# Kernel optimization log

Hardware: AMD Instinct MI355X
Metric: run time of the kernel (lower is better)

The kernel has to match this reference:

```python
import jax, jax.numpy as jnp
import numpy as np

DIM = 1024
NUM_HEADS = 16
HEAD_DIM = DIM // NUM_HEADS
SCALE = HEAD_DIM ** -0.5


def setup_inputs() -> dict:
    key = jax.random.key(0)
    k1, k2, k3 = jax.random.split(key, 3)
    B, S = 2, 2048
    x = jax.random.normal(k1, (B, S, DIM), dtype=jnp.float32)
    # nn.Linear(dim, 3*dim, bias=False): store as [in, out] for x @ W
    w_qkv = jax.random.normal(k2, (DIM, 3 * DIM), dtype=jnp.float32) * (DIM ** -0.5)
    w_out = jax.random.normal(k3, (DIM, DIM), dtype=jnp.float32) * (DIM ** -0.5)
    return {"x": x, "w_qkv": w_qkv, "w_out": w_out}


def reference(x, w_qkv, w_out):
    B, S, _ = x.shape
    qkv = x @ w_qkv                               # [B,S,3*D]
    q, k, v = jnp.split(qkv, 3, axis=-1)          # each [B,S,D]
    def heads(t):
        return t.reshape(B, S, NUM_HEADS, HEAD_DIM).transpose(0, 2, 1, 3)  # [B,H,S,d]
    q, k, v = heads(q), heads(k), heads(v)
    scores = jnp.einsum('bhqd,bhkd->bhqk', q, k) * SCALE   # [B,H,S,S]
    probs = jax.nn.softmax(scores, axis=-1)
    out = jnp.einsum('bhqk,bhkd->bhqd', probs, v)          # [B,H,S,d]
    out = out.transpose(0, 2, 1, 3).reshape(B, S, DIM)
    return out @ w_out
```

## Files before the change

### kernel.cpp

```cpp
#include <hip/hip_runtime.h>


typedef __bf16 bf16x8 __attribute__((ext_vector_type(8)));
typedef __bf16 bf16x4 __attribute__((ext_vector_type(4)));
typedef float floatx4 __attribute__((ext_vector_type(4)));

#define MFMA16(a, b, c) __builtin_amdgcn_mfma_f32_16x16x32_bf16((a), (b), (c), 0, 0, 0)

#if defined(__has_builtin)
#if __has_builtin(__builtin_amdgcn_exp2f)
#define EXP2F __builtin_amdgcn_exp2f
#endif
#endif
#ifndef EXP2F
#define EXP2F exp2f
#endif

__device__ __forceinline__ unsigned pk_bf16(float a, float b) {
  unsigned r;
  asm("v_cvt_pk_bf16_f32 %0, %1, %2" : "=v"(r) : "v"(a), "v"(b));
  return r;
}

__device__ __forceinline__ void gl_lds16(const void* g, void* l) {
  __builtin_amdgcn_global_load_lds((__attribute__((address_space(1))) void*)(g),
                                   (__attribute__((address_space(3))) void*)(l),
                                   16, 0, 0);
}

__global__ __launch_bounds__(256) void prep(const float* __restrict__ x,
                                            const float* __restrict__ w_qkv,
                                            const float* __restrict__ w_out,
                                            __bf16* __restrict__ xb,
                                            __bf16* __restrict__ wqkvt,
                                            __bf16* __restrict__ woutt) {
  __shared__ float tile[64][65];
  const int bid = blockIdx.x, t = threadIdx.x;
  if (bid < 4096) {
    int i = (bid * 256 + t) * 4;
    float4 v = *(const float4*)(x + i);
    bf16x4 o = { (__bf16)v.x, (__bf16)v.y, (__bf16)v.z, (__bf16)v.w };
    *(bf16x4*)(xb + i) = o;
    return;
  }
  const float* w;
  __bf16* wt;
  int K = 1024, N, k0, n0;
  if (bid < 4864) {
    int i = bid - 4096;
    w = w_qkv; wt = wqkvt; N = 3072; k0 = (i & 15) * 64; n0 = (i >> 4) * 64;
  } else {
    int i = bid - 4864;
    w = w_out; wt = woutt; N = 1024; k0 = (i & 15) * 64; n0 = (i >> 4) * 64;
  }
  for (int j = 0; j < 16; ++j) {
    int e = j * 256 + t, r = e >> 6, c = e & 63;
    tile[r][c] = w[(size_t)(k0 + r) * N + n0 + c];
  }
  __syncthreads();
  for (int j = 0; j < 16; ++j) {
    int e = j * 256 + t, r = e >> 6, c = e & 63;
    wt[(size_t)(n0 + r) * K + k0 + c] = (__bf16)tile[c][r];
  }
}

__global__ __launch_bounds__(256) void gemm_qkv(const __bf16* __restrict__ A,
                                                const __bf16* __restrict__ Bt,
                                                __bf16* __restrict__ qkb,
                                                __bf16* __restrict__ vt) {
  constexpr int K = 1024;
  constexpr float QSCALE = 0.18033688f;
  __shared__ __align__(16) __bf16 aS[128 * 32];
  __shared__ __align__(16) __bf16 bS[128 * 32];
  const int t = threadIdx.x;
  const int lane = t & 63, wave = t >> 6;
  const int l15 = lane & 15, quad = lane >> 4;
  const int wm = wave >> 1, wn = wave & 1;
  const int m0 = blockIdx.y * 128, n0 = blockIdx.x * 128;

  const floatx4 fzero = {0.f, 0.f, 0.f, 0.f};
  floatx4 acc[4][4];
  for (int mt = 0; mt < 4; ++mt)
    for (int nt = 0; nt < 4; ++nt) acc[mt][nt] = fzero;

  const int arow = t >> 2;
  const int ach = ((t & 3) ^ (arow & 3)) * 8;
  const __bf16* gA0 = A + (size_t)(m0 + arow) * K + ach;
  const __bf16* gA1 = gA0 + (size_t)64 * K;
  const __bf16* gB0 = Bt + (size_t)(n0 + arow) * K + ach;
  const __bf16* gB1 = gB0 + (size_t)64 * K;
  const int swz = (quad ^ (l15 & 3)) * 8;

  for (int k0 = 0; k0 < K; k0 += 32) {
    __syncthreads();
    gl_lds16(gA0 + k0, (char*)aS + t * 16);
    gl_lds16(gA1 + k0, (char*)aS + 4096 + t * 16);
    gl_lds16(gB0 + k0, (char*)bS + t * 16);
    gl_lds16(gB1 + k0, (char*)bS + 4096 + t * 16);
    __syncthreads();

    bf16x8 af[4], bfr[4];
    for (int mt = 0; mt < 4; ++mt)
      af[mt] = *(const bf16x8*)(aS + (wm * 64 + mt * 16 + l15) * 32 + swz);
    for (int nt = 0; nt < 4; ++nt)
      bfr[nt] = *(const bf16x8*)(bS + (wn * 64 + nt * 16 + l15) * 32 + swz);
    for (int mt = 0; mt < 4; ++mt)
      for (int nt = 0; nt < 4; ++nt)
        acc[mt][nt] = MFMA16(af[mt], bfr[nt], acc[mt][nt]);
  }

  for (int mt = 0; mt < 4; ++mt) {
    int row = m0 + wm * 64 + mt * 16 + quad * 4;
    for (int nt = 0; nt < 4; ++nt) {
      int col0 = n0 + wn * 64 + nt * 16;
      if (col0 >= 2048) {
        int dfull = col0 + l15 - 2048;
        int bh = ((row >> 11) << 4) + (dfull >> 6);
        int d = dfull & 63, s0 = row & 2047;
        bf16x4 pk = { (__bf16)acc[mt][nt][0], (__bf16)acc[mt][nt][1],
                      (__bf16)acc[mt][nt][2], (__bf16)acc[mt][nt][3] };
        *(bf16x4*)(vt + ((size_t)bh * 64 + d) * 2048 + s0) = pk;
      } else {
        float sc = (col0 < 1024) ? QSCALE : 1.0f;
        int col = col0 + l15;
        __bf16* cp = qkb + (size_t)row * 2048 + col;
        for (int r = 0; r < 4; ++r) cp[(size_t)r * 2048] = (__bf16)(acc[mt][nt][r] * sc);
      }
    }
  }
}

__global__ __launch_bounds__(256) void gemm_n64(const __bf16* __restrict__ A,
                                                const __bf16* __restrict__ Bt,
                                                float* __restrict__ C) {
  constexpr int K = 1024, N = 1024;
  __shared__ __align__(16) __bf16 aS[128 * 32];
  __shared__ __align__(16) __bf16 bS[64 * 32];
  const int t = threadIdx.x;
  const int lane = t & 63, wave = t >> 6;
  const int l15 = lane & 15, quad = lane >> 4;
  const int m0 = blockIdx.y * 128, n0 = blockIdx.x * 64;

  const floatx4 fzero = {0.f, 0.f, 0.f, 0.f};
  floatx4 acc[2][4];
  for (int mt = 0; mt < 2; ++mt)
    for (int nt = 0; nt < 4; ++nt) acc[mt][nt] = fzero;

  const int arow = t >> 2;
  const int ach = ((t & 3) ^ (arow & 3)) * 8;
  const __bf16* gA0 = A + (size_t)(m0 + arow) * K + ach;
  const __bf16* gA1 = gA0 + (size_t)64 * K;
  const __bf16* gB0 = Bt + (size_t)(n0 + arow) * K + ach;
  const int swz = (quad ^ (l15 & 3)) * 8;

  for (int k0 = 0; k0 < K; k0 += 32) {
    __syncthreads();
    gl_lds16(gA0 + k0, (char*)aS + t * 16);
    gl_lds16(gA1 + k0, (char*)aS + 4096 + t * 16);
    gl_lds16(gB0 + k0, (char*)bS + t * 16);
    __syncthreads();

    bf16x8 af[2], bfr[4];
    for (int mt = 0; mt < 2; ++mt)
      af[mt] = *(const bf16x8*)(aS + (wave * 32 + mt * 16 + l15) * 32 + swz);
    for (int nt = 0; nt < 4; ++nt)
      bfr[nt] = *(const bf16x8*)(bS + (nt * 16 + l15) * 32 + swz);
    for (int mt = 0; mt < 2; ++mt)
      for (int nt = 0; nt < 4; ++nt)
        acc[mt][nt] = MFMA16(af[mt], bfr[nt], acc[mt][nt]);
  }

  for (int mt = 0; mt < 2; ++mt) {
    int row = m0 + wave * 32 + mt * 16 + quad * 4;
    for (int nt = 0; nt < 4; ++nt) {
      int col = n0 + nt * 16 + l15;
      float* cp = C + (size_t)row * N + col;
      for (int r = 0; r < 4; ++r) cp[(size_t)r * N] = acc[mt][nt][r];
    }
  }
}

__global__ __launch_bounds__(256, 2) void flash_attn(const __bf16* __restrict__ qkb,
                                                     const __bf16* __restrict__ vt,
                                                     __bf16* __restrict__ out) {
  __shared__ __align__(16) __bf16 kS[2 * 64 * 64];
  __shared__ __align__(16) __bf16 vS[2 * 64 * 64];

  const int t = threadIdx.x;
  const int lane = t & 63, wave = t >> 6;
  const int l15 = lane & 15, quad = lane >> 4;
  const int id = blockIdx.x;
  const int xcd = id & 7, slot = id >> 3;
  const int bh = xcd * 4 + (slot >> 4), qb = slot & 15;
  const int b = bh >> 4, h = bh & 15;

  bf16x8 qf[2][2];
  for (int qt = 0; qt < 2; ++qt) {
    const __bf16* qp = qkb +
        (size_t)(b * 2048 + qb * 128 + wave * 32 + qt * 16 + l15) * 2048 + h * 64 + quad * 8;
    qf[qt][0] = *(const bf16x8*)qp;
    qf[qt][1] = *(const bf16x8*)(qp + 32);
  }

  bf16x8 onef;
  for (int j = 0; j < 8; ++j) onef[j] = (__bf16)1.0f;

  const floatx4 fzero = {0.f, 0.f, 0.f, 0.f};
  floatx4 oacc[2][4], lacc[2];
  for (int qt = 0; qt < 2; ++qt) {
    lacc[qt] = fzero;
    for (int dt = 0; dt < 4; ++dt) oacc[qt][dt] = fzero;
  }

  const int srow = t >> 3, schk = (t & 7) ^ (srow & 7);
  const __bf16* kg0 =
      qkb + (size_t)(b * 2048 + srow) * 2048 + 1024 + h * 64 + schk * 8;
  const __bf16* kg1 = kg0 + (size_t)32 * 2048;
  const __bf16* vg0 =
      vt + (size_t)bh * 64 * 2048 + (size_t)srow * 2048 + schk * 8;
  const __bf16* vg1 = vg0 + (size_t)32 * 2048;

  const int l7 = l15 & 7;

  gl_lds16(kg0, (char*)kS + t * 16);
  gl_lds16(kg1, (char*)kS + 4096 + t * 16);
  gl_lds16(vg0, (char*)vS + t * 16);
  gl_lds16(vg1, (char*)vS + 4096 + t * 16);

  for (int nb = 0; nb < 32; ++nb) {
    __syncthreads();

    if (nb < 31) {
      const size_t n1 = (size_t)(nb + 1) * 64;
      const int oB = ((nb + 1) & 1) * 8192;
      gl_lds16(kg0 + n1 * 2048, (char*)kS + oB + t * 16);
      gl_lds16(kg1 + n1 * 2048, (char*)kS + oB + 4096 + t * 16);
      gl_lds16(vg0 + n1, (char*)vS + oB + t * 16);
      gl_lds16(vg1 + n1, (char*)vS + oB + 4096 + t * 16);
    }

    const __bf16* kC = kS + (nb & 1) * 4096;
    const __bf16* vC = vS + (nb & 1) * 4096;

    bf16x8 kf[4][2];
    for (int nt = 0; nt < 4; ++nt)
      for (int ks = 0; ks < 2; ++ks)
        kf[nt][ks] = *(const bf16x8*)(kC + (nt * 16 + l15) * 64 +
                                      ((ks * 4 + quad) ^ l7) * 8);
    bf16x8 vf[2][4];
    for (int ks = 0; ks < 2; ++ks)
      for (int dt = 0; dt < 4; ++dt)
        vf[ks][dt] = *(const bf16x8*)(vC + (dt * 16 + l15) * 64 +
                                      ((ks * 4 + quad) ^ l7) * 8);

    floatx4 sa[2][4];
    __builtin_amdgcn_s_setprio(1);
    for (int qt = 0; qt < 2; ++qt)
      for (int nt = 0; nt < 4; ++nt) {
        floatx4 a = fzero;
        a = MFMA16(kf[nt][0], qf[qt][0], a);
        a = MFMA16(kf[nt][1], qf[qt][1], a);
        sa[qt][nt] = a;
      }
    __builtin_amdgcn_s_setprio(0);

    for (int qt = 0; qt < 2; ++qt) {
      bf16x8 pa[2];
      for (int ks = 0; ks < 2; ++ks) {
        const int n0 = 2 * ks, n1 = 2 * ks + 1;
        float e00 = EXP2F(sa[qt][n0][0]), e01 = EXP2F(sa[qt][n0][1]);
        float e02 = EXP2F(sa[qt][n0][2]), e03 = EXP2F(sa[qt][n0][3]);
        float e10 = EXP2F(sa[qt][n1][0]), e11 = EXP2F(sa[qt][n1][1]);
        float e12 = EXP2F(sa[qt][n1][2]), e13 = EXP2F(sa[qt][n1][3]);
        unsigned x0 = pk_bf16(e00, e01), x1 = pk_bf16(e02, e03);
        unsigned y0 = pk_bf16(e10, e11), y1 = pk_bf16(e12, e13);
        unsigned d0 = x0, d2 = y0;
        asm("v_permlane32_swap_b32 %0, %1" : "+v"(d0), "+v"(d2));
        asm("v_permlane16_swap_b32 %0, %1" : "+v"(d0), "+v"(d2));
        unsigned d1 = x1, d3 = y1;
        asm("v_permlane32_swap_b32 %0, %1" : "+v"(d1), "+v"(d3));
        asm("v_permlane16_swap_b32 %0, %1" : "+v"(d1), "+v"(d3));
        union { unsigned u[4]; bf16x8 v8; } pu;
        pu.u[0] = d0; pu.u[1] = d1; pu.u[2] = d2; pu.u[3] = d3;
        pa[ks] = pu.v8;
      }
      __builtin_amdgcn_s_setprio(1);
      for (int ks = 0; ks < 2; ++ks) {
        for (int dt = 0; dt < 4; ++dt)
          oacc[qt][dt] = MFMA16(pa[ks], vf[ks][dt], oacc[qt][dt]);
        lacc[qt] = MFMA16(pa[ks], onef, lacc[qt]);
      }
      __builtin_amdgcn_s_setprio(0);
    }
  }

  for (int qt = 0; qt < 2; ++qt) {
    float inv[4];
    for (int r = 0; r < 4; ++r) inv[r] = 1.f / lacc[qt][r];
    __bf16* ob = out +
        (size_t)(b * 2048 + qb * 128 + wave * 32 + qt * 16 + quad * 4) * 1024 + h * 64;
    for (int dt = 0; dt < 4; ++dt)
      for (int r = 0; r < 4; ++r)
        ob[(size_t)r * 1024 + dt * 16 + l15] = (__bf16)(oacc[qt][dt][r] * inv[r]);
  }
}

extern "C" void kernel_launch(void* const* d_in, const int* in_sizes, int n_in,
                              void* d_out, int out_size, void* d_ws, size_t ws_size,
                              hipStream_t stream) {
  const float* x = (const float*)d_in[0];
  const float* w_qkv = (const float*)d_in[1];
  const float* w_out = (const float*)d_in[2];
  float* out = (float*)d_out;

  char* ws = (char*)d_ws;
  __bf16* xb = (__bf16*)(ws);
  __bf16* wqkvt = (__bf16*)(ws + ((size_t)8 << 20));
  __bf16* qkb = (__bf16*)(ws + ((size_t)16 << 20));
  __bf16* vtg = (__bf16*)(ws + ((size_t)32 << 20));
  __bf16* aout = (__bf16*)(ws + ((size_t)40 << 20));
  __bf16* woutt = (__bf16*)(ws + ((size_t)48 << 20));

  prep<<<5120, 256, 0, stream>>>(x, w_qkv, w_out, xb, wqkvt, woutt);
  gemm_qkv<<<dim3(24, 32), 256, 0, stream>>>(xb, wqkvt, qkb, vtg);
  flash_attn<<<512, 256, 0, stream>>>(qkb, vtg, aout);
  gemm_n64<<<dim3(16, 32), 256, 0, stream>>>(aout, woutt, out);
}
```

Before: 173.8 us.

## Split attention KV range across two blocks and merge with combine kernel

Each attention block now processes half of the key/value sequence, which doubles the grid to 1024 blocks and raises the occupancy hint to 4 blocks per CU. Unnormalised fp16 partial outputs and fp32 row sums go to workspace buffers. A new combine kernel adds the two partials, divides by the summed denominators and writes bf16 in place into the buffer the output GEMM reads. This aims to fill more of the CUs and hide latency, at the cost of an extra launch, extra memory traffic, and a risk of fp16 range or precision loss in the unnormalised partials.

Result: slower. 248.4 us (+43.0%).

```diff
diff --git a/kernel.cpp b/kernel.cpp
--- a/kernel.cpp
+++ b/kernel.cpp
@@ -4,6 +4,7 @@
 typedef __bf16 bf16x8 __attribute__((ext_vector_type(8)));
 typedef __bf16 bf16x4 __attribute__((ext_vector_type(4)));
 typedef float floatx4 __attribute__((ext_vector_type(4)));
+typedef _Float16 f16x8 __attribute__((ext_vector_type(8)));
 
 #define MFMA16(a, b, c) __builtin_amdgcn_mfma_f32_16x16x32_bf16((a), (b), (c), 0, 0, 0)
 
@@ -180,9 +181,12 @@
   }
 }
 
-__global__ __launch_bounds__(256, 2) void flash_attn(const __bf16* __restrict__ qkb,
+__global__ __launch_bounds__(256, 4) void flash_attn(const __bf16* __restrict__ qkb,
                                                      const __bf16* __restrict__ vt,
-                                                     __bf16* __restrict__ out) {
+                                                     _Float16* __restrict__ o0,
+                                                     _Float16* __restrict__ o1,
+                                                     float* __restrict__ l0,
+                                                     float* __restrict__ l1) {
   __shared__ __align__(16) __bf16 kS[2 * 64 * 64];
   __shared__ __align__(16) __bf16 vS[2 * 64 * 64];
 
@@ -190,9 +194,10 @@
   const int lane = t & 63, wave = t >> 6;
   const int l15 = lane & 15, quad = lane >> 4;
   const int id = blockIdx.x;
-  const int xcd = id & 7, slot = id >> 3;
-  const int bh = xcd * 4 + (slot >> 4), qb = slot & 15;
+  const int xcd = id & 7, r = id >> 3;
+  const int bh = xcd * 4 + (r >> 5), qb = (r >> 1) & 15, g = r & 1;
   const int b = bh >> 4, h = bh & 15;
+  const int kofs = g << 10;
 
   bf16x8 qf[2][2];
   for (int qt = 0; qt < 2; ++qt) {
@@ -214,10 +219,10 @@
 
   const int srow = t >> 3, schk = (t & 7) ^ (srow & 7);
   const __bf16* kg0 =
-      qkb + (size_t)(b * 2048 + srow) * 2048 + 1024 + h * 64 + schk * 8;
+      qkb + (size_t)(b * 2048 + kofs + srow) * 2048 + 1024 + h * 64 + schk * 8;
   const __bf16* kg1 = kg0 + (size_t)32 * 2048;
   const __bf16* vg0 =
-      vt + (size_t)bh * 64 * 2048 + (size_t)srow * 2048 + schk * 8;
+      vt + (size_t)bh * 64 * 2048 + (size_t)srow * 2048 + kofs + schk * 8;
   const __bf16* vg1 = vg0 + (size_t)32 * 2048;
 
   const int l7 = l15 & 7;
@@ -227,10 +232,10 @@
   gl_lds16(vg0, (char*)vS + t * 16);
   gl_lds16(vg1, (char*)vS + 4096 + t * 16);
 
-  for (int nb = 0; nb < 32; ++nb) {
-    __syncthreads();
-
-    if (nb < 31) {
+  for (int nb = 0; nb < 16; ++nb) {
+    __syncthreads();
+
+    if (nb < 15) {
       const size_t n1 = (size_t)(nb + 1) * 64;
       const int oB = ((nb + 1) & 1) * 8192;
       gl_lds16(kg0 + n1 * 2048, (char*)kS + oB + t * 16);
@@ -294,15 +299,34 @@
     }
   }
 
+  _Float16* og = g ? o1 : o0;
+  float* lg = g ? l1 : l0;
   for (int qt = 0; qt < 2; ++qt) {
-    float inv[4];
-    for (int r = 0; r < 4; ++r) inv[r] = 1.f / lacc[qt][r];
-    __bf16* ob = out +
-        (size_t)(b * 2048 + qb * 128 + wave * 32 + qt * 16 + quad * 4) * 1024 + h * 64;
+    const int row0 = b * 2048 + qb * 128 + wave * 32 + qt * 16 + quad * 4;
+    _Float16* op = og + (size_t)row0 * 1024 + h * 64;
     for (int dt = 0; dt < 4; ++dt)
-      for (int r = 0; r < 4; ++r)
-        ob[(size_t)r * 1024 + dt * 16 + l15] = (__bf16)(oacc[qt][dt][r] * inv[r]);
-  }
+      for (int r2 = 0; r2 < 4; ++r2)
+        op[(size_t)r2 * 1024 + dt * 16 + l15] = (_Float16)oacc[qt][dt][r2];
+    if (l15 == 0) {
+      float* lp = lg + (size_t)row0 * 16 + h;
+      for (int r2 = 0; r2 < 4; ++r2) lp[(size_t)r2 * 16] = lacc[qt][r2];
+    }
+  }
+}
+
+__global__ __launch_bounds__(256) void combine(const _Float16* __restrict__ o0,
+                                               _Float16* __restrict__ o1,
+                                               const float* __restrict__ l0,
+                                               const float* __restrict__ l1) {
+  const size_t i = ((size_t)blockIdx.x * 256 + threadIdx.x) * 8;
+  f16x8 a = *(const f16x8*)(o0 + i);
+  f16x8 c = *(const f16x8*)(o1 + i);
+  const int li = (int)(i >> 6);
+  const float inv = 1.0f / (l0[li] + l1[li]);
+  bf16x8 res;
+  for (int j = 0; j < 8; ++j)
+    res[j] = (__bf16)(((float)a[j] + (float)c[j]) * inv);
+  *(bf16x8*)((__bf16*)o1 + i) = res;
 }
 
 extern "C" void kernel_launch(void* const* d_in, const int* in_sizes, int n_in,
@@ -315,14 +339,19 @@
 
   char* ws = (char*)d_ws;
   __bf16* xb = (__bf16*)(ws);
+  _Float16* o0 = (_Float16*)(ws);
   __bf16* wqkvt = (__bf16*)(ws + ((size_t)8 << 20));
+  float* l0 = (float*)(ws + ((size_t)14 << 20));
+  float* l1 = (float*)(ws + ((size_t)14 << 20) + 262144);
   __bf16* qkb = (__bf16*)(ws + ((size_t)16 << 20));
   __bf16* vtg = (__bf16*)(ws + ((size_t)32 << 20));
+  _Float16* o1 = (_Float16*)(ws + ((size_t)40 << 20));
   __bf16* aout = (__bf16*)(ws + ((size_t)40 << 20));
   __bf16* woutt = (__bf16*)(ws + ((size_t)48 << 20));
 
   prep<<<5120, 256, 0, stream>>>(x, w_qkv, w_out, xb, wqkvt, woutt);
   gemm_qkv<<<dim3(24, 32), 256, 0, stream>>>(xb, wqkvt, qkb, vtg);
-  flash_attn<<<512, 256, 0, stream>>>(qkb, vtg, aout);
+  flash_attn<<<1024, 256, 0, stream>>>(qkb, vtg, o0, o1, l0, l1);
+  combine<<<2048, 256, 0, stream>>>(o0, o1, l0, l1);
   gemm_n64<<<dim3(16, 32), 256, 0, stream>>>(aout, woutt, out);
 }
```

## Software-pipeline attention loop to overlap next-tile QK with softmax and PV

Applied to the files above, without the earlier changes.

Restructures the attention inner loop into a two-stage software pipeline. The QK^T MFMAs for the next key tile are issued while the exp/pack softmax and PV MFMAs of the current tile run, using ping-pong score and V-fragment register sets and a manually unrolled loop with prologue and epilogue. The goal is to hide VALU exp and permlane latency behind matrix-core work. In exchange it needs more registers, which may reduce occupancy or cause spills.

New measurement: 172.9 us, median of 2. Within noise of the previous version (-0.5%).

```diff
diff --git a/kernel.cpp b/kernel.cpp
--- a/kernel.cpp
+++ b/kernel.cpp
@@ -222,38 +222,33 @@
 
   const int l7 = l15 & 7;
 
-  gl_lds16(kg0, (char*)kS + t * 16);
-  gl_lds16(kg1, (char*)kS + 4096 + t * 16);
-  gl_lds16(vg0, (char*)vS + t * 16);
-  gl_lds16(vg1, (char*)vS + 4096 + t * 16);
-
-  for (int nb = 0; nb < 32; ++nb) {
-    __syncthreads();
-
-    if (nb < 31) {
-      const size_t n1 = (size_t)(nb + 1) * 64;
-      const int oB = ((nb + 1) & 1) * 8192;
-      gl_lds16(kg0 + n1 * 2048, (char*)kS + oB + t * 16);
-      gl_lds16(kg1 + n1 * 2048, (char*)kS + oB + 4096 + t * 16);
-      gl_lds16(vg0 + n1, (char*)vS + oB + t * 16);
-      gl_lds16(vg1 + n1, (char*)vS + oB + 4096 + t * 16);
-    }
-
-    const __bf16* kC = kS + (nb & 1) * 4096;
-    const __bf16* vC = vS + (nb & 1) * 4096;
-
-    bf16x8 kf[4][2];
+  bf16x8 kf[4][2];
+  bf16x8 vfA[2][4], vfB[2][4];
+  floatx4 saA[2][4], saB[2][4];
+
+  auto stage = [&](int tile) {
+    const size_t n1 = (size_t)tile * 64;
+    const int oB = (tile & 1) * 8192;
+    gl_lds16(kg0 + n1 * 2048, (char*)kS + oB + t * 16);
+    gl_lds16(kg1 + n1 * 2048, (char*)kS + oB + 4096 + t * 16);
+    gl_lds16(vg0 + n1, (char*)vS + oB + t * 16);
+    gl_lds16(vg1 + n1, (char*)vS + oB + 4096 + t * 16);
+  };
+
+  auto loadKV = [&](int buf, bf16x8 (&vf)[2][4]) {
+    const __bf16* kC = kS + buf * 4096;
+    const __bf16* vC = vS + buf * 4096;
     for (int nt = 0; nt < 4; ++nt)
       for (int ks = 0; ks < 2; ++ks)
         kf[nt][ks] = *(const bf16x8*)(kC + (nt * 16 + l15) * 64 +
                                       ((ks * 4 + quad) ^ l7) * 8);
-    bf16x8 vf[2][4];
     for (int ks = 0; ks < 2; ++ks)
       for (int dt = 0; dt < 4; ++dt)
         vf[ks][dt] = *(const bf16x8*)(vC + (dt * 16 + l15) * 64 +
                                       ((ks * 4 + quad) ^ l7) * 8);
-
-    floatx4 sa[2][4];
+  };
+
+  auto qk = [&](floatx4 (&sa)[2][4]) {
     __builtin_amdgcn_s_setprio(1);
     for (int qt = 0; qt < 2; ++qt)
       for (int nt = 0; nt < 4; ++nt) {
@@ -263,7 +258,9 @@
         sa[qt][nt] = a;
       }
     __builtin_amdgcn_s_setprio(0);
-
+  };
+
+  auto smpv = [&](floatx4 (&sa)[2][4], bf16x8 (&vf)[2][4]) {
     for (int qt = 0; qt < 2; ++qt) {
       bf16x8 pa[2];
       for (int ks = 0; ks < 2; ++ks) {
@@ -292,7 +289,32 @@
       }
       __builtin_amdgcn_s_setprio(0);
     }
-  }
+  };
+
+  stage(0);
+  __syncthreads();
+  stage(1);
+  loadKV(0, vfA);
+  qk(saA);
+
+  for (int nb = 1; nb < 31; nb += 2) {
+    __syncthreads();
+    stage(nb + 1);
+    loadKV(1, vfB);
+    smpv(saA, vfA);
+    qk(saB);
+    __syncthreads();
+    stage(nb + 2);
+    loadKV(0, vfA);
+    smpv(saB, vfB);
+    qk(saA);
+  }
+
+  __syncthreads();
+  loadKV(1, vfB);
+  smpv(saA, vfA);
+  qk(saB);
+  smpv(saB, vfB);
 
   for (int qt = 0; qt < 2; ++qt) {
     float inv[4];
```

## Software-pipeline flash attention with 4-deep LDS ring and staggered QK/softmax-PV

Applied to the files above, without the earlier changes.

The K/V shared-memory ring grows from 2 to 4 tiles, so two tiles are staged per barrier instead of one, halving the number of __syncthreads. The main loop is restructured so the QK^T MFMAs of the next tile are issued alongside the exp/softmax and PV work of the previous one, using double register sets for scores and V fragments. The goal is to hide LDS latency and exp latency behind MFMA work. The costs are double the LDS per block and extra live registers, which could reduce occupancy or cause spills.

Measured after the change: 172.1 us. About the same (-1.0%).

```diff
diff --git a/kernel.cpp b/kernel.cpp
--- a/kernel.cpp
+++ b/kernel.cpp
@@ -183,8 +183,8 @@
 __global__ __launch_bounds__(256, 2) void flash_attn(const __bf16* __restrict__ qkb,
                                                      const __bf16* __restrict__ vt,
                                                      __bf16* __restrict__ out) {
-  __shared__ __align__(16) __bf16 kS[2 * 64 * 64];
-  __shared__ __align__(16) __bf16 vS[2 * 64 * 64];
+  __shared__ __align__(16) __bf16 kS[4 * 64 * 64];
+  __shared__ __align__(16) __bf16 vS[4 * 64 * 64];
 
   const int t = threadIdx.x;
   const int lane = t & 63, wave = t >> 6;
@@ -222,38 +222,35 @@
 
   const int l7 = l15 & 7;
 
-  gl_lds16(kg0, (char*)kS + t * 16);
-  gl_lds16(kg1, (char*)kS + 4096 + t * 16);
-  gl_lds16(vg0, (char*)vS + t * 16);
-  gl_lds16(vg1, (char*)vS + 4096 + t * 16);
-
-  for (int nb = 0; nb < 32; ++nb) {
-    __syncthreads();
-
-    if (nb < 31) {
-      const size_t n1 = (size_t)(nb + 1) * 64;
-      const int oB = ((nb + 1) & 1) * 8192;
-      gl_lds16(kg0 + n1 * 2048, (char*)kS + oB + t * 16);
-      gl_lds16(kg1 + n1 * 2048, (char*)kS + oB + 4096 + t * 16);
-      gl_lds16(vg0 + n1, (char*)vS + oB + t * 16);
-      gl_lds16(vg1 + n1, (char*)vS + oB + 4096 + t * 16);
-    }
-
-    const __bf16* kC = kS + (nb & 1) * 4096;
-    const __bf16* vC = vS + (nb & 1) * 4096;
-
-    bf16x8 kf[4][2];
+  bf16x8 kf[4][2];
+  bf16x8 vfC[2][4], vfT[2][4];
+  floatx4 saC[2][4], saT[2][4];
+
+  auto stage = [&](int tile) {
+    const size_t n1 = (size_t)tile * 64;
+    const int oB = (tile & 3) * 8192;
+    gl_lds16(kg0 + n1 * 2048, (char*)kS + oB + t * 16);
+    gl_lds16(kg1 + n1 * 2048, (char*)kS + oB + 4096 + t * 16);
+    gl_lds16(vg0 + n1, (char*)vS + oB + t * 16);
+    gl_lds16(vg1 + n1, (char*)vS + oB + 4096 + t * 16);
+  };
+
+  auto loadK = [&](int tile) {
+    const __bf16* kC = kS + (tile & 3) * 4096;
     for (int nt = 0; nt < 4; ++nt)
       for (int ks = 0; ks < 2; ++ks)
         kf[nt][ks] = *(const bf16x8*)(kC + (nt * 16 + l15) * 64 +
                                       ((ks * 4 + quad) ^ l7) * 8);
-    bf16x8 vf[2][4];
+  };
+  auto loadV = [&](int tile, bf16x8 (&vf)[2][4]) {
+    const __bf16* vC = vS + (tile & 3) * 4096;
     for (int ks = 0; ks < 2; ++ks)
       for (int dt = 0; dt < 4; ++dt)
         vf[ks][dt] = *(const bf16x8*)(vC + (dt * 16 + l15) * 64 +
                                       ((ks * 4 + quad) ^ l7) * 8);
-
-    floatx4 sa[2][4];
+  };
+
+  auto qk = [&](floatx4 (&sa)[2][4]) {
     __builtin_amdgcn_s_setprio(1);
     for (int qt = 0; qt < 2; ++qt)
       for (int nt = 0; nt < 4; ++nt) {
@@ -263,7 +260,9 @@
         sa[qt][nt] = a;
       }
     __builtin_amdgcn_s_setprio(0);
-
+  };
+
+  auto smpv = [&](floatx4 (&sa)[2][4], bf16x8 (&vf)[2][4]) {
     for (int qt = 0; qt < 2; ++qt) {
       bf16x8 pa[2];
       for (int ks = 0; ks < 2; ++ks) {
@@ -292,7 +291,39 @@
       }
       __builtin_amdgcn_s_setprio(0);
     }
-  }
+  };
+
+  stage(0); stage(1);
+  __syncthreads();
+  stage(2); stage(3);
+  loadK(0);
+  qk(saT);
+  loadV(0, vfT); loadK(1);
+  smpv(saT, vfT);
+  qk(saC);
+  loadV(1, vfC);
+
+  for (int s = 1; s < 15; ++s) {
+    __syncthreads();
+    stage(2 * s + 2); stage(2 * s + 3);
+    loadK(2 * s);
+    smpv(saC, vfC);
+    qk(saT);
+    loadV(2 * s, vfT); loadK(2 * s + 1);
+    smpv(saT, vfT);
+    qk(saC);
+    loadV(2 * s + 1, vfC);
+  }
+
+  __syncthreads();
+  loadK(30);
+  smpv(saC, vfC);
+  qk(saT);
+  loadV(30, vfT); loadK(31);
+  smpv(saT, vfT);
+  qk(saC);
+  loadV(31, vfC);
+  smpv(saC, vfC);
 
   for (int qt = 0; qt < 2; ++qt) {
     float inv[4];
```
